# Optimization experiments

Measured on AMD Instinct MI355X. Metric: run time of the kernel, lower is better.

Reference implementation:

```python
import jax, jax.numpy as jnp
import numpy as np

N_NODES = 50000
N_EDGES = 800000
IN_DIM, HID_DIM, N_CLASS = 128, 128, 2
DROPOUT_P = 0.5
NEG_SLOPE = 0.01  # F.leaky_relu default


def gcn_conv(x, src, dst, W, b, n_nodes):
    """PyG GCNConv: add self-loops, sym-normalize, aggregate, then bias."""
    loops = jnp.arange(n_nodes, dtype=src.dtype)
    s = jnp.concatenate([src, loops])
    d = jnp.concatenate([dst, loops])
    # degree on A + I (edge weights = 1), counted at destination
    deg = jax.ops.segment_sum(jnp.ones_like(d, dtype=x.dtype), d, num_segments=n_nodes)
    dis = jnp.where(deg > 0, jax.lax.rsqrt(deg), 0.0)  # deg^{-1/2}
    norm = dis[s] * dis[d]                               # [E+N]
    h = x @ W                                            # [N, out]
    msg = h[s] * norm[:, None]                           # gather + scale
    out = jax.ops.segment_sum(msg, d, num_segments=n_nodes)  # scatter-add
    return out + b


def dropout(x, p, key):
    keep = 1.0 - p
    mask = jax.random.bernoulli(key, keep, x.shape)
    return jnp.where(mask, x / keep, 0.0)


def setup_inputs() -> dict:
    key = jax.random.key(0)
    ks = jax.random.split(key, 8)
    x = jax.random.normal(ks[0], (N_NODES, IN_DIM), dtype=jnp.float32)
    edge_index = jax.random.randint(ks[1], (2, N_EDGES), 0, N_NODES, dtype=jnp.int64)
    def glorot(k, fin, fout):
        lim = np.sqrt(6.0 / (fin + fout)).astype(np.float32)
        return jax.random.uniform(k, (fin, fout), jnp.float32, -lim, lim)
    W1 = glorot(ks[2], IN_DIM, HID_DIM)
    W2 = glorot(ks[3], HID_DIM, HID_DIM)
    W3 = glorot(ks[4], HID_DIM, N_CLASS)
    b1 = jnp.zeros((HID_DIM,), jnp.float32)
    b2 = jnp.zeros((HID_DIM,), jnp.float32)
    b3 = jnp.zeros((N_CLASS,), jnp.float32)
    return {"x": x, "edge_index": edge_index, "W1": W1, "b1": b1,
            "W2": W2, "b2": b2, "W3": W3, "b3": b3}


def reference(x, edge_index, W1, b1, W2, b2, W3, b3):
    src, dst = edge_index[0], edge_index[1]
    n = x.shape[0]
    dkey = jax.random.key(42)
    k1, k2 = jax.random.split(dkey)
    h = gcn_conv(x, src, dst, W1, b1, n)
    h = jax.nn.leaky_relu(h, NEG_SLOPE)
    h = dropout(h, DROPOUT_P, k1)
    h = gcn_conv(h, src, dst, W2, b2, n)
    h = jax.nn.leaky_relu(h, NEG_SLOPE)
    h = dropout(h, DROPOUT_P, k2)
    h = gcn_conv(h, src, dst, W3, b3, n)
    return jax.nn.log_softmax(h, axis=1)
```

## Files before the change

### kernel.cpp

```cpp
#include <hip/hip_runtime.h>
#include <stdint.h>

#define N_NODES 50000
#define N_EDGES 800000
#define DIM     128
#define TOT     (N_NODES * DIM)
#define NB   196
#define CAP  8192
#define CHUNK 2048
#define NBLK 391
#define GCAP 4096
#define G3CAP 8192
#define XBLKS (TOT / 4 / 256)

typedef __attribute__((ext_vector_type(8))) unsigned short ushort8_t;
typedef __attribute__((ext_vector_type(8))) short bfrag;
typedef __attribute__((ext_vector_type(4))) float f32x4;

__host__ __device__ inline void threefry2x32(uint32_t k0, uint32_t k1,
                                             uint32_t x0, uint32_t x1,
                                             uint32_t& o0, uint32_t& o1) {
    uint32_t ks0 = k0, ks1 = k1, ks2 = k0 ^ k1 ^ 0x1BD11BDAu;
    uint32_t v0 = x0 + ks0, v1 = x1 + ks1;
#define TF_R(r) { v0 += v1; v1 = (v1 << (r)) | (v1 >> (32 - (r))); v1 ^= v0; }
    TF_R(13) TF_R(15) TF_R(26) TF_R(6)
    v0 += ks1; v1 += ks2 + 1u;
    TF_R(17) TF_R(29) TF_R(16) TF_R(24)
    v0 += ks2; v1 += ks0 + 2u;
    TF_R(13) TF_R(15) TF_R(26) TF_R(6)
    v0 += ks0; v1 += ks1 + 3u;
    TF_R(17) TF_R(29) TF_R(16) TF_R(24)
    v0 += ks1; v1 += ks2 + 4u;
    TF_R(13) TF_R(15) TF_R(26) TF_R(6)
    v0 += ks2; v1 += ks0 + 5u;
#undef TF_R
    o0 = v0; o1 = v1;
}

__device__ inline float drop_scale(uint32_t kk0, uint32_t kk1, uint32_t i) {
    uint32_t b0, b1;
    threefry2x32(kk0, kk1, 0u, i, b0, b1);
    uint32_t bits = b0 ^ b1;
    return (bits >> 31) ? 0.0f : 2.0f;
}

__device__ inline float bf2f(ushort u) {
    return __uint_as_float(((uint32_t)u) << 16);
}
__device__ inline float bfpair_lo(uint32_t u) { return __uint_as_float(u << 16); }
__device__ inline float bfpair_hi(uint32_t u) { return __uint_as_float(u & 0xffff0000u); }

__device__ inline ushort f2bf_rne(float f) {
    uint32_t bits = __float_as_uint(f);
    uint32_t lsb = (bits >> 16) & 1u;
    bits += 0x7fffu + lsb;
    return (ushort)(bits >> 16);
}

__device__ inline void gemm_body(const ushort* __restrict__ Xb,
                                 const ushort* __restrict__ Wt,
                                 const float* __restrict__ dis,
                                 ushort* __restrict__ Hb, int gb, int tid) {
    int w = tid >> 6, lane = tid & 63;
    int m0 = gb * 128 + w * 32;
    int lrow = lane & 15, quad = lane >> 4;
    f32x4 acc[2][8] = {};
    for (int kt = 0; kt < DIM; kt += 32) {
        bfrag a[2], b[8];
        #pragma unroll
        for (int t = 0; t < 2; ++t) {
            int m = m0 + t * 16 + lrow;
            if (m >= N_NODES) m = 0;
            a[t] = *(const bfrag*)(Xb + (size_t)m * DIM + kt + quad * 8);
        }
        #pragma unroll
        for (int c = 0; c < 8; ++c) {
            int n = c * 16 + lrow;
            b[c] = *(const bfrag*)(Wt + (size_t)n * DIM + kt + quad * 8);
        }
        #pragma unroll
        for (int t = 0; t < 2; ++t)
            #pragma unroll
            for (int c = 0; c < 8; ++c)
                acc[t][c] = __builtin_amdgcn_mfma_f32_16x16x32_bf16(a[t], b[c], acc[t][c], 0, 0, 0);
    }
    #pragma unroll
    for (int t = 0; t < 2; ++t) {
        #pragma unroll
        for (int r = 0; r < 4; ++r) {
            int rowi = m0 + t * 16 + quad * 4 + r;
            if (rowi < N_NODES) {
                float dv = dis[rowi];
                #pragma unroll
                for (int c = 0; c < 8; ++c) {
                    int feat = c * 16 + lrow;
                    int fp = feat >> 5, off = feat & 31;
                    Hb[((size_t)fp * N_NODES + rowi) * 32 + off] = f2bf_rne(acc[t][c][r] * dv);
                }
            }
        }
    }
}

__global__ __launch_bounds__(256) void k_prep(const float* __restrict__ x,
                                              const float* __restrict__ W1,
                                              const float* __restrict__ W2,
                                              ushort* __restrict__ Xb,
                                              ushort* __restrict__ W1t,
                                              ushort* __restrict__ W2t,
                                              const int* __restrict__ src,
                                              const int* __restrict__ dst,
                                              uint32_t* __restrict__ gcur,
                                              uint32_t* __restrict__ packed) {
    __shared__ uint32_t h[NB];
    int b = blockIdx.x;
    int t = threadIdx.x;
    if (b < NBLK) {
        int sb = b;
        if (t < NB) h[t] = 0u;
        __syncthreads();
        int base = sb * CHUNK;
        #pragma unroll
        for (int i = 0; i < CHUNK / 256; ++i) {
            int e = base + i * 256 + t;
            if (e < N_EDGES) atomicAdd(&h[((uint32_t)dst[e]) >> 8], 1u);
        }
        __syncthreads();
        if (t < NB) {
            uint32_t c = h[t];
            h[t] = c ? atomicAdd(&gcur[t], c) : 0u;
        }
        __syncthreads();
        #pragma unroll
        for (int i = 0; i < CHUNK / 256; ++i) {
            int e = base + i * 256 + t;
            if (e < N_EDGES) {
                uint32_t d = (uint32_t)dst[e];
                uint32_t s = (uint32_t)src[e];
                uint32_t bk = d >> 8;
                uint32_t pos = atomicAdd(&h[bk], 1u);
                if (pos < CAP)
                    packed[(size_t)bk * CAP + pos] = ((d & 255u) << 16) | s;
            }
        }
    } else if (b < NBLK + 128) {
        int j = (b - NBLK) * 256 + t;
        const float* W = (j < DIM * DIM) ? W1 : W2;
        ushort* Wt = (j < DIM * DIM) ? W1t : W2t;
        int i = j & (DIM * DIM - 1);
        int k = i >> 7, n = i & 127;
        Wt[n * DIM + k] = f2bf_rne(W[k * DIM + n]);
    } else {
        int i = (b - NBLK - 128) * 256 + t;
        float4 v = ((const float4*)x)[i];
        ushort4 o;
        o.x = f2bf_rne(v.x); o.y = f2bf_rne(v.y);
        o.z = f2bf_rne(v.z); o.w = f2bf_rne(v.w);
        ((ushort4*)Xb)[i] = o;
    }
}

__global__ __launch_bounds__(256) void k_fill(const uint32_t* __restrict__ gcur,
                                              const uint32_t* __restrict__ packed,
                                              uint32_t* __restrict__ row,
                                              float* __restrict__ dis,
                                              ushort* __restrict__ col16) {
    __shared__ uint32_t sdeg[256];
    __shared__ uint32_t scan[256];
    __shared__ uint32_t cur[256];
    int b = blockIdx.x;
    int t = threadIdx.x;
    uint32_t n = gcur[b];
    scan[t] = (t < b) ? gcur[t] : 0u;
    __syncthreads();
    for (int off = 1; off < 256; off <<= 1) {
        uint32_t x = (t >= off) ? scan[t - off] : 0u;
        __syncthreads();
        scan[t] += x;
        __syncthreads();
    }
    uint32_t cbase = scan[255];
    __syncthreads();
    uint32_t pbase = (uint32_t)b * CAP;
    sdeg[t] = 0u;
    __syncthreads();
    uint32_t mine[24]; int cnt = 0;
    for (uint32_t i = t; i < n; i += 256) {
        uint32_t u = packed[pbase + i];
        mine[cnt++] = u;
        atomicAdd(&sdeg[u >> 16], 1u);
    }
    __syncthreads();
    uint32_t myd = sdeg[t];
    scan[t] = myd;
    __syncthreads();
    for (int off = 1; off < 256; off <<= 1) {
        uint32_t x = (t >= off) ? scan[t - off] : 0u;
        __syncthreads();
        scan[t] += x;
        __syncthreads();
    }
    uint32_t excl = scan[t] - myd;
    cur[t] = excl;
    int v = b * 256 + t;
    if (v <= N_NODES) row[v] = cbase + excl;
    if (v < N_NODES)  dis[v] = 1.0f / sqrtf((float)(myd + 1u));
    __syncthreads();
    for (int j = 0; j < cnt; ++j) {
        uint32_t u = mine[j];
        uint32_t pos = cbase + atomicAdd(&cur[u >> 16], 1u);
        col16[pos] = (ushort)(u & 0xffffu);
    }
}

__global__ __launch_bounds__(256) void k_gather(const uint32_t* __restrict__ row,
                                                const ushort* __restrict__ col16,
                                                const float* __restrict__ dis,
                                                const ushort* __restrict__ Hb,
                                                const float* __restrict__ bias,
                                                ushort* __restrict__ OUTb,
                                                uint32_t kk0, uint32_t kk1) {
    __shared__ ushort scol[GCAP];
    __shared__ uint32_t srow[65];
    int fp = blockIdx.x & 3;
    int c = blockIdx.x >> 2;
    int tid = threadIdx.x;
    int nbase = c * 64;
    int nend = nbase + 64; if (nend > N_NODES) nend = N_NODES;
    int nloc = nend - nbase;
    for (int i = tid; i <= nloc; i += 256) srow[i] = row[nbase + i];
    __syncthreads();
    uint32_t eLo = srow[0];
    uint32_t count = srow[nloc] - eLo;
    bool staged = count <= GCAP;
    if (staged) {
        for (uint32_t i = tid; i < count; i += 256) scol[i] = col16[eLo + i];
    }
    __syncthreads();

    int nl = tid >> 2;
    int q  = tid & 3;
    int v = nbase + nl;
    if (v >= N_NODES) return;
    const ushort* Hf = Hb + (size_t)fp * N_NODES * 32;
    ushort8_t hv = *((const ushort8_t*)(Hf + (size_t)v * 32 + q * 8));
    float acc[8];
    #pragma unroll
    for (int j = 0; j < 8; ++j) acc[j] = bf2f(hv[j]);

    uint32_t e0 = srow[nl] - eLo, e1 = srow[nl + 1] - eLo;
    uint32_t e = e0;
    if (staged) {
        for (; e + 4 <= e1; e += 4) {
            uint32_t s0 = scol[e], s1 = scol[e + 1], s2 = scol[e + 2], s3 = scol[e + 3];
            ushort8_t h0 = *((const ushort8_t*)(Hf + (size_t)s0 * 32 + q * 8));
            ushort8_t h1 = *((const ushort8_t*)(Hf + (size_t)s1 * 32 + q * 8));
            ushort8_t h2 = *((const ushort8_t*)(Hf + (size_t)s2 * 32 + q * 8));
            ushort8_t h3 = *((const ushort8_t*)(Hf + (size_t)s3 * 32 + q * 8));
            #pragma unroll
            for (int j = 0; j < 8; ++j)
                acc[j] += (bf2f(h0[j]) + bf2f(h1[j])) + (bf2f(h2[j]) + bf2f(h3[j]));
        }
        for (; e < e1; ++e) {
            uint32_t s0 = scol[e];
            ushort8_t h0 = *((const ushort8_t*)(Hf + (size_t)s0 * 32 + q * 8));
            #pragma unroll
            for (int j = 0; j < 8; ++j) acc[j] += bf2f(h0[j]);
        }
    } else {
        for (; e < e1; ++e) {
            uint32_t s0 = col16[eLo + e];
            ushort8_t h0 = *((const ushort8_t*)(Hf + (size_t)s0 * 32 + q * 8));
            #pragma unroll
            for (int j = 0; j < 8; ++j) acc[j] += bf2f(h0[j]);
        }
    }

    float dv = dis[v];
    int cbase = fp * 32 + q * 8;
    uint32_t ibase = (uint32_t)(v * DIM + cbase);
    ushort8_t o;
    #pragma unroll
    for (int j = 0; j < 8; ++j) {
        float z = acc[j] * dv + bias[cbase + j];
        z = (z >= 0.f) ? z : 0.01f * z;
        z *= drop_scale(kk0, kk1, ibase + j);
        o[j] = f2bf_rne(z);
    }
    *((ushort8_t*)(OUTb + (size_t)v * DIM + cbase)) = o;
}

__global__ __launch_bounds__(256) void k_gemm_mfma(const ushort* __restrict__ Xb,
                                                   const ushort* __restrict__ Wt,
                                                   const float* __restrict__ dis,
                                                   ushort* __restrict__ Hb) {
    gemm_body(Xb, Wt, dis, Hb, blockIdx.x, threadIdx.x);
}

__global__ void k_gemm_cls(const ushort* __restrict__ Bb, const float* __restrict__ W3,
                           const float* __restrict__ dis, float* __restrict__ O) {
    int v = blockIdx.x * blockDim.x + threadIdx.x;
    if (v >= N_NODES) return;
    const uint32_t* r = (const uint32_t*)(Bb + (size_t)v * DIM);
    float a0 = 0.f, a1 = 0.f;
#pragma unroll 8
    for (int w = 0; w < 64; ++w) {
        uint32_t u = r[w];
        float x0 = bfpair_lo(u), x1 = bfpair_hi(u);
        const float* wp = W3 + w * 4;
        a0 += x0 * wp[0] + x1 * wp[2];
        a1 += x0 * wp[1] + x1 * wp[3];
    }
    float dv = dis[v];
    O[v * 2 + 0] = a0 * dv;
    O[v * 2 + 1] = a1 * dv;
}

__global__ __launch_bounds__(256) void k_gather3(const uint32_t* __restrict__ row,
                                                 const ushort* __restrict__ col16,
                                                 const float* __restrict__ dis,
                                                 const float* __restrict__ H3s,
                                                 const float* __restrict__ b3,
                                                 float* __restrict__ out) {
    __shared__ ushort scol[G3CAP];
    __shared__ uint32_t srow[257];
    int tid = threadIdx.x;
    int nbase = blockIdx.x * 256;
    int nend = nbase + 256; if (nend > N_NODES) nend = N_NODES;
    int nloc = nend - nbase;
    for (int i = tid; i <= nloc; i += 256) srow[i] = row[nbase + i];
    __syncthreads();
    uint32_t eLo = srow[0];
    uint32_t count = srow[nloc] - eLo;
    bool staged = count <= G3CAP;
    if (staged) {
        for (uint32_t i = tid; i < count; i += 256) scol[i] = col16[eLo + i];
    }
    __syncthreads();

    int v = nbase + tid;
    if (v >= N_NODES) return;
    const float2* H2 = (const float2*)H3s;
    float2 h = H2[v];
    float z0 = h.x, z1 = h.y;
    uint32_t e0 = srow[tid] - eLo, e1 = srow[tid + 1] - eLo;
    uint32_t e = e0;
    if (staged) {
        for (; e + 2 <= e1; e += 2) {
            float2 ha = H2[scol[e]];
            float2 hb = H2[scol[e + 1]];
            z0 += ha.x + hb.x; z1 += ha.y + hb.y;
        }
        if (e < e1) {
            float2 ha = H2[scol[e]];
            z0 += ha.x; z1 += ha.y;
        }
    } else {
        for (; e < e1; ++e) {
            float2 ha = H2[col16[eLo + e]];
            z0 += ha.x; z1 += ha.y;
        }
    }
    float dv = dis[v];
    z0 = z0 * dv + b3[0];
    z1 = z1 * dv + b3[1];
    float m = fmaxf(z0, z1);
    float lse = m + logf(expf(z0 - m) + expf(z1 - m));
    out[v * 2 + 0] = z0 - lse;
    out[v * 2 + 1] = z1 - lse;
}

extern "C" void kernel_launch(void* const* d_in, const int* in_sizes, int n_in,
                              void* d_out, int out_size, void* d_ws, size_t ws_size,
                              hipStream_t stream) {
    const float* x  = (const float*)d_in[0];
    const int*   ei = (const int*)d_in[1];
    const float* W1 = (const float*)d_in[2];
    const float* b1 = (const float*)d_in[3];
    const float* W2 = (const float*)d_in[4];
    const float* b2 = (const float*)d_in[5];
    const float* W3 = (const float*)d_in[6];
    const float* b3 = (const float*)d_in[7];
    float* out = (float*)d_out;

    const int* src = ei;
    const int* dst = ei + N_EDGES;

    uint32_t* wsu = (uint32_t*)d_ws;
    float*    wsf = (float*)d_ws;
    uint32_t* gcur   = wsu;
    uint32_t* row    = wsu + 256;
    float*    dis    = wsf + 50304;
    uint32_t* packed = wsu + 100352;
    ushort*   col16  = (ushort*)(wsu + 1705984);
    ushort*   Hb     = (ushort*)(wsu + 2106112);
    ushort*   Xb     = (ushort*)(wsu + 5306112);
    ushort*   Bb     = (ushort*)(wsu + 8506112);
    ushort*   W1t    = (ushort*)(wsu + 11706112);
    ushort*   W2t    = (ushort*)(wsu + 11714304);
    float*    h3s    = wsf + 11722496;

    uint32_t k1a, k1b, k2a, k2b;
    threefry2x32(0u, 42u, 0u, 0u, k1a, k1b);
    threefry2x32(0u, 42u, 0u, 1u, k2a, k2b);

    hipMemsetAsync(gcur, 0, 256 * sizeof(uint32_t), stream);

    k_prep<<<NBLK + 128 + XBLKS, 256, 0, stream>>>(x, W1, W2, Xb, W1t, W2t,
                                                   src, dst, gcur, packed);

    k_fill<<<NB, 256, 0, stream>>>(gcur, packed, row, dis, col16);

    int mgrid = (N_NODES + 127) / 128;
    int ggrid = ((N_NODES + 63) / 64) * 4;

    k_gemm_mfma<<<mgrid, 256, 0, stream>>>(Xb, W1t, dis, Hb);
    k_gather<<<ggrid, 256, 0, stream>>>(row, col16, dis, Hb, b1, Bb, k1a, k1b);

    k_gemm_mfma<<<mgrid, 256, 0, stream>>>(Bb, W2t, dis, Hb);
    k_gather<<<ggrid, 256, 0, stream>>>(row, col16, dis, Hb, b2, Bb, k2a, k2b);

    k_gemm_cls<<<(N_NODES + 255) / 256, 256, 0, stream>>>(Bb, W3, dis, h3s);
    k_gather3<<<(N_NODES + 255) / 256, 256, 0, stream>>>(row, col16, dis, h3s, b3, out);
}
```

Before: 231.9 us.

## Fuse x bf16 conversion into GEMM1 and classifier GEMM into second gather

The first GEMM now reads fp32 x directly and converts to bf16 in registers, which removes the separate conversion pass and the Xb buffer. The second gather kernel now applies the W3 projection in its epilogue, reducing with shuffles and accumulating into h3s with atomics. This drops the Bb write/read and the k_gemm_cls launch, at the cost of an extra memset and per-node atomics. k_prep keeps edge indices in registers instead of reloading them, and k_fill re-reads packed instead of holding a private array, which lowers register pressure.

```diff
diff --git a/kernel.cpp b/kernel.cpp
--- a/kernel.cpp
+++ b/kernel.cpp
@@ -4,14 +4,12 @@
 #define N_NODES 50000
 #define N_EDGES 800000
 #define DIM     128
-#define TOT     (N_NODES * DIM)
 #define NB   196
 #define CAP  8192
 #define CHUNK 2048
 #define NBLK 391
 #define GCAP 4096
 #define G3CAP 8192
-#define XBLKS (TOT / 4 / 256)
 
 typedef __attribute__((ext_vector_type(8))) unsigned short ushort8_t;
 typedef __attribute__((ext_vector_type(8))) short bfrag;
@@ -47,8 +45,6 @@
 __device__ inline float bf2f(ushort u) {
     return __uint_as_float(((uint32_t)u) << 16);
 }
-__device__ inline float bfpair_lo(uint32_t u) { return __uint_as_float(u << 16); }
-__device__ inline float bfpair_hi(uint32_t u) { return __uint_as_float(u & 0xffff0000u); }
 
 __device__ inline ushort f2bf_rne(float f) {
     uint32_t bits = __float_as_uint(f);
@@ -57,7 +53,9 @@
     return (ushort)(bits >> 16);
 }
 
+template<int F32A>
 __device__ inline void gemm_body(const ushort* __restrict__ Xb,
+                                 const float* __restrict__ Xf,
                                  const ushort* __restrict__ Wt,
                                  const float* __restrict__ dis,
                                  ushort* __restrict__ Hb, int gb, int tid) {
@@ -71,7 +69,18 @@
         for (int t = 0; t < 2; ++t) {
             int m = m0 + t * 16 + lrow;
             if (m >= N_NODES) m = 0;
-            a[t] = *(const bfrag*)(Xb + (size_t)m * DIM + kt + quad * 8);
+            if (F32A) {
+                const float* p = Xf + (size_t)m * DIM + kt + quad * 8;
+                f32x4 v0 = *(const f32x4*)p;
+                f32x4 v1 = *(const f32x4*)(p + 4);
+                #pragma unroll
+                for (int j = 0; j < 4; ++j) {
+                    a[t][j]     = (short)f2bf_rne(v0[j]);
+                    a[t][j + 4] = (short)f2bf_rne(v1[j]);
+                }
+            } else {
+                a[t] = *(const bfrag*)(Xb + (size_t)m * DIM + kt + quad * 8);
+            }
         }
         #pragma unroll
         for (int c = 0; c < 8; ++c) {
@@ -102,10 +111,8 @@
     }
 }
 
-__global__ __launch_bounds__(256) void k_prep(const float* __restrict__ x,
-                                              const float* __restrict__ W1,
+__global__ __launch_bounds__(256) void k_prep(const float* __restrict__ W1,
                                               const float* __restrict__ W2,
-                                              ushort* __restrict__ Xb,
                                               ushort* __restrict__ W1t,
                                               ushort* __restrict__ W2t,
                                               const int* __restrict__ src,
@@ -116,14 +123,20 @@
     int b = blockIdx.x;
     int t = threadIdx.x;
     if (b < NBLK) {
-        int sb = b;
+        uint32_t dc[CHUNK / 256], sc[CHUNK / 256];
         if (t < NB) h[t] = 0u;
         __syncthreads();
-        int base = sb * CHUNK;
+        int base = b * CHUNK;
         #pragma unroll
         for (int i = 0; i < CHUNK / 256; ++i) {
             int e = base + i * 256 + t;
-            if (e < N_EDGES) atomicAdd(&h[((uint32_t)dst[e]) >> 8], 1u);
+            if (e < N_EDGES) {
+                dc[i] = (uint32_t)dst[e];
+                sc[i] = (uint32_t)src[e];
+                atomicAdd(&h[dc[i] >> 8], 1u);
+            } else {
+                dc[i] = 0xffffffffu;
+            }
         }
         __syncthreads();
         if (t < NB) {
@@ -133,30 +146,22 @@
         __syncthreads();
         #pragma unroll
         for (int i = 0; i < CHUNK / 256; ++i) {
-            int e = base + i * 256 + t;
-            if (e < N_EDGES) {
-                uint32_t d = (uint32_t)dst[e];
-                uint32_t s = (uint32_t)src[e];
+            if (dc[i] != 0xffffffffu) {
+                uint32_t d = dc[i];
+                uint32_t s = sc[i];
                 uint32_t bk = d >> 8;
                 uint32_t pos = atomicAdd(&h[bk], 1u);
                 if (pos < CAP)
                     packed[(size_t)bk * CAP + pos] = ((d & 255u) << 16) | s;
             }
         }
-    } else if (b < NBLK + 128) {
+    } else {
         int j = (b - NBLK) * 256 + t;
         const float* W = (j < DIM * DIM) ? W1 : W2;
         ushort* Wt = (j < DIM * DIM) ? W1t : W2t;
         int i = j & (DIM * DIM - 1);
         int k = i >> 7, n = i & 127;
         Wt[n * DIM + k] = f2bf_rne(W[k * DIM + n]);
-    } else {
-        int i = (b - NBLK - 128) * 256 + t;
-        float4 v = ((const float4*)x)[i];
-        ushort4 o;
-        o.x = f2bf_rne(v.x); o.y = f2bf_rne(v.y);
-        o.z = f2bf_rne(v.z); o.w = f2bf_rne(v.w);
-        ((ushort4*)Xb)[i] = o;
     }
 }
 
@@ -184,10 +189,8 @@
     uint32_t pbase = (uint32_t)b * CAP;
     sdeg[t] = 0u;
     __syncthreads();
-    uint32_t mine[24]; int cnt = 0;
     for (uint32_t i = t; i < n; i += 256) {
         uint32_t u = packed[pbase + i];
-        mine[cnt++] = u;
         atomicAdd(&sdeg[u >> 16], 1u);
     }
     __syncthreads();
@@ -206,20 +209,23 @@
     if (v <= N_NODES) row[v] = cbase + excl;
     if (v < N_NODES)  dis[v] = 1.0f / sqrtf((float)(myd + 1u));
     __syncthreads();
-    for (int j = 0; j < cnt; ++j) {
-        uint32_t u = mine[j];
+    for (uint32_t i = t; i < n; i += 256) {
+        uint32_t u = packed[pbase + i];
         uint32_t pos = cbase + atomicAdd(&cur[u >> 16], 1u);
         col16[pos] = (ushort)(u & 0xffffu);
     }
 }
 
-__global__ __launch_bounds__(256) void k_gather(const uint32_t* __restrict__ row,
-                                                const ushort* __restrict__ col16,
-                                                const float* __restrict__ dis,
-                                                const ushort* __restrict__ Hb,
-                                                const float* __restrict__ bias,
-                                                ushort* __restrict__ OUTb,
-                                                uint32_t kk0, uint32_t kk1) {
+template<int CLS>
+__global__ __launch_bounds__(256) void k_gather_t(const uint32_t* __restrict__ row,
+                                                  const ushort* __restrict__ col16,
+                                                  const float* __restrict__ dis,
+                                                  const ushort* __restrict__ Hb,
+                                                  const float* __restrict__ bias,
+                                                  ushort* __restrict__ OUTb,
+                                                  const float* __restrict__ W3,
+                                                  float* __restrict__ h3s,
+                                                  uint32_t kk0, uint32_t kk1) {
     __shared__ ushort scol[GCAP];
     __shared__ uint32_t srow[65];
     int fp = blockIdx.x & 3;
@@ -279,41 +285,46 @@
     float dv = dis[v];
     int cbase = fp * 32 + q * 8;
     uint32_t ibase = (uint32_t)(v * DIM + cbase);
-    ushort8_t o;
-    #pragma unroll
-    for (int j = 0; j < 8; ++j) {
-        float z = acc[j] * dv + bias[cbase + j];
-        z = (z >= 0.f) ? z : 0.01f * z;
-        z *= drop_scale(kk0, kk1, ibase + j);
-        o[j] = f2bf_rne(z);
-    }
-    *((ushort8_t*)(OUTb + (size_t)v * DIM + cbase)) = o;
-}
-
-__global__ __launch_bounds__(256) void k_gemm_mfma(const ushort* __restrict__ Xb,
+    if (CLS == 0) {
+        ushort8_t o;
+        #pragma unroll
+        for (int j = 0; j < 8; ++j) {
+            float z = acc[j] * dv + bias[cbase + j];
+            z = (z >= 0.f) ? z : 0.01f * z;
+            z *= drop_scale(kk0, kk1, ibase + j);
+            o[j] = f2bf_rne(z);
+        }
+        *((ushort8_t*)(OUTb + (size_t)v * DIM + cbase)) = o;
+    } else {
+        float o0 = 0.f, o1 = 0.f;
+        #pragma unroll
+        for (int j = 0; j < 8; ++j) {
+            float z = acc[j] * dv + bias[cbase + j];
+            z = (z >= 0.f) ? z : 0.01f * z;
+            z *= drop_scale(kk0, kk1, ibase + j);
+            o0 += z * W3[(cbase + j) * 2 + 0];
+            o1 += z * W3[(cbase + j) * 2 + 1];
+        }
+        o0 += __shfl_xor(o0, 1); o0 += __shfl_xor(o0, 2);
+        o1 += __shfl_xor(o1, 1); o1 += __shfl_xor(o1, 2);
+        if (q == 0) {
+            atomicAdd(&h3s[v * 2 + 0], o0 * dv);
+            atomicAdd(&h3s[v * 2 + 1], o1 * dv);
+        }
+    }
+}
+
+__global__ __launch_bounds__(256) void k_gemm_f32(const float* __restrict__ Xf,
+                                                  const ushort* __restrict__ Wt,
+                                                  const float* __restrict__ dis,
+                                                  ushort* __restrict__ Hb) {
+    gemm_body<1>(nullptr, Xf, Wt, dis, Hb, blockIdx.x, threadIdx.x);
+}
+__global__ __launch_bounds__(256) void k_gemm_bf16(const ushort* __restrict__ Xb,
                                                    const ushort* __restrict__ Wt,
                                                    const float* __restrict__ dis,
                                                    ushort* __restrict__ Hb) {
-    gemm_body(Xb, Wt, dis, Hb, blockIdx.x, threadIdx.x);
-}
-
-__global__ void k_gemm_cls(const ushort* __restrict__ Bb, const float* __restrict__ W3,
-                           const float* __restrict__ dis, float* __restrict__ O) {
-    int v = blockIdx.x * blockDim.x + threadIdx.x;
-    if (v >= N_NODES) return;
-    const uint32_t* r = (const uint32_t*)(Bb + (size_t)v * DIM);
-    float a0 = 0.f, a1 = 0.f;
-#pragma unroll 8
-    for (int w = 0; w < 64; ++w) {
-        uint32_t u = r[w];
-        float x0 = bfpair_lo(u), x1 = bfpair_hi(u);
-        const float* wp = W3 + w * 4;
-        a0 += x0 * wp[0] + x1 * wp[2];
-        a1 += x0 * wp[1] + x1 * wp[3];
-    }
-    float dv = dis[v];
-    O[v * 2 + 0] = a0 * dv;
-    O[v * 2 + 1] = a1 * dv;
+    gemm_body<0>(Xb, nullptr, Wt, dis, Hb, blockIdx.x, threadIdx.x);
 }
 
 __global__ __launch_bounds__(256) void k_gather3(const uint32_t* __restrict__ row,
@@ -394,7 +405,6 @@
     uint32_t* packed = wsu + 100352;
     ushort*   col16  = (ushort*)(wsu + 1705984);
     ushort*   Hb     = (ushort*)(wsu + 2106112);
-    ushort*   Xb     = (ushort*)(wsu + 5306112);
     ushort*   Bb     = (ushort*)(wsu + 8506112);
     ushort*   W1t    = (ushort*)(wsu + 11706112);
     ushort*   W2t    = (ushort*)(wsu + 11714304);
@@ -405,21 +415,23 @@
     threefry2x32(0u, 42u, 0u, 1u, k2a, k2b);
 
     hipMemsetAsync(gcur, 0, 256 * sizeof(uint32_t), stream);
-
-    k_prep<<<NBLK + 128 + XBLKS, 256, 0, stream>>>(x, W1, W2, Xb, W1t, W2t,
-                                                   src, dst, gcur, packed);
+    hipMemsetAsync(h3s, 0, N_NODES * 2 * sizeof(float), stream);
+
+    k_prep<<<NBLK + 128, 256, 0, stream>>>(W1, W2, W1t, W2t,
+                                           src, dst, gcur, packed);
 
     k_fill<<<NB, 256, 0, stream>>>(gcur, packed, row, dis, col16);
 
     int mgrid = (N_NODES + 127) / 128;
     int ggrid = ((N_NODES + 63) / 64) * 4;
 
-    k_gemm_mfma<<<mgrid, 256, 0, stream>>>(Xb, W1t, dis, Hb);
-    k_gather<<<ggrid, 256, 0, stream>>>(row, col16, dis, Hb, b1, Bb, k1a, k1b);
-
-    k_gemm_mfma<<<mgrid, 256, 0, stream>>>(Bb, W2t, dis, Hb);
-    k_gather<<<ggrid, 256, 0, stream>>>(row, col16, dis, Hb, b2, Bb, k2a, k2b);
-
-    k_gemm_cls<<<(N_NODES + 255) / 256, 256, 0, stream>>>(Bb, W3, dis, h3s);
+    k_gemm_f32<<<mgrid, 256, 0, stream>>>(x, W1t, dis, Hb);
+    k_gather_t<0><<<ggrid, 256, 0, stream>>>(row, col16, dis, Hb, b1, Bb,
+                                             nullptr, nullptr, k1a, k1b);
+
+    k_gemm_bf16<<<mgrid, 256, 0, stream>>>(Bb, W2t, dis, Hb);
+    k_gather_t<1><<<ggrid, 256, 0, stream>>>(row, col16, dis, Hb, b2, nullptr,
+                                             W3, h3s, k2a, k2b);
+
     k_gather3<<<(N_NODES + 255) / 256, 256, 0, stream>>>(row, col16, dis, h3s, b3, out);
 }
```

Result: faster. 223.6 us (-3.6%).
